# Kernel optimization log

Hardware: AMD Instinct MI355X
Metric: run time of the kernel (lower is better)

Reference implementation:

```python
import jax, jax.numpy as jnp
import numpy as np

EMB = 1024
HEADS = 16
HEAD_SZ = EMB // HEADS
EPS = 1e-5


def _layernorm(x, g, b):
    mu = jnp.mean(x, axis=-1, keepdims=True)
    var = jnp.mean(jnp.square(x - mu), axis=-1, keepdims=True)
    return (x - mu) * jax.lax.rsqrt(var + EPS) * g + b


def setup_inputs() -> dict:
    key = jax.random.key(0)
    ks = jax.random.split(key, 12)
    s_in = 1.0 / np.sqrt(EMB)
    s_h = 1.0 / np.sqrt(4 * EMB)
    return {
        "x": jax.random.normal(ks[0], (4, 1024, EMB), jnp.float32),
        # per-head Q/K/V projections stacked: [H, EMB, HEAD_SZ], no bias
        "wq": jax.random.normal(ks[1], (HEADS, EMB, HEAD_SZ), jnp.float32) * s_in,
        "wk": jax.random.normal(ks[2], (HEADS, EMB, HEAD_SZ), jnp.float32) * s_in,
        "wv": jax.random.normal(ks[3], (HEADS, EMB, HEAD_SZ), jnp.float32) * s_in,
        "w_proj": jax.random.normal(ks[4], (EMB, EMB), jnp.float32) * s_in,
        "b_proj": jnp.zeros((EMB,), jnp.float32),
        "w1": jax.random.normal(ks[5], (EMB, 4 * EMB), jnp.float32) * s_in,
        "b1": jnp.zeros((4 * EMB,), jnp.float32),
        "w2": jax.random.normal(ks[6], (4 * EMB, EMB), jnp.float32) * s_h,
        "b2": jnp.zeros((EMB,), jnp.float32),
        "g1": jnp.ones((EMB,), jnp.float32),
        "be1": jnp.zeros((EMB,), jnp.float32),
        "g2": jnp.ones((EMB,), jnp.float32),
        "be2": jnp.zeros((EMB,), jnp.float32),
    }


def reference(x, wq, wk, wv, w_proj, b_proj, w1, b1, w2, b2, g1, be1, g2, be2):
    B, T, C = x.shape
    # --- self-attention (pre-norm) ---
    h = _layernorm(x, g1, be1)
    q = jnp.einsum("btc,hcd->bhtd", h, wq)
    k = jnp.einsum("btc,hcd->bhtd", h, wk)
    v = jnp.einsum("btc,hcd->bhtd", h, wv)
    scale = 1.0 / jnp.sqrt(jnp.asarray(HEAD_SZ, x.dtype))
    scores = jnp.einsum("bhtd,bhsd->bhts", q, k) * scale  # non-causal: SDPA called with no mask
    attn = jax.nn.softmax(scores, axis=-1)
    o = jnp.einsum("bhts,bhsd->bhtd", attn, v)
    o = o.transpose(0, 2, 1, 3).reshape(B, T, C)  # concat heads (same order as torch.cat)
    sa_out = o @ w_proj + b_proj
    x = x + sa_out
    # --- feed-forward; note ln2 applied twice, faithful to source ---
    t = _layernorm(x, g2, be2)
    t = _layernorm(t, g2, be2)
    ff = jax.nn.relu(t @ w1 + b1) @ w2 + b2
    return x + ff
```

## Files before the change

kernel.cpp:

```cpp
#include <hip/hip_runtime.h>
#include <hip/hip_bf16.h>
#include <math.h>
#include <stdint.h>

typedef __bf16 bf16_t;
typedef __bf16 bf16x4 __attribute__((ext_vector_type(4)));
typedef __bf16 bf16x8 __attribute__((ext_vector_type(8)));
typedef float floatx4 __attribute__((ext_vector_type(4)));

#define BM 128
#define BK 32

__device__ __forceinline__ void gload16(const void* g, void* lds) {
    __builtin_amdgcn_global_load_lds(
        (__attribute__((address_space(1))) void*)(uintptr_t)g,
        (__attribute__((address_space(3))) void*)(uintptr_t)lds,
        16, 0, 0);
}

__global__ void transpose_all(const float* __restrict__ wq, const float* __restrict__ wk,
                              const float* __restrict__ wv, const float* __restrict__ w_proj,
                              const float* __restrict__ w1, const float* __restrict__ w2,
                              bf16_t* __restrict__ WQKVT, bf16_t* __restrict__ WPROJT,
                              bf16_t* __restrict__ W1T, bf16_t* __restrict__ W2T)
{
    const int idx = blockIdx.x;
    const float* in; bf16_t* out; int R, C, rt, ct;
    if (idx < 768) {
        const int z = idx >> 8;
        const int hd = (idx >> 4) & 15;
        rt = idx & 15; ct = 0; R = 1024; C = 64;
        in  = (z == 0 ? wq : z == 1 ? wk : wv) + hd * 65536;
        out = WQKVT + z * (1 << 20) + hd * 65536;
    } else if (idx < 1024) {
        const int t = idx - 768; rt = t & 15; ct = t >> 4; R = 1024; C = 1024;
        in = w_proj; out = WPROJT;
    } else if (idx < 2048) {
        const int t = idx - 1024; rt = t & 15; ct = t >> 4; R = 1024; C = 4096;
        in = w1; out = W1T;
    } else {
        const int t = idx - 2048; rt = t & 63; ct = t >> 6; R = 4096; C = 1024;
        in = w2; out = W2T;
    }
    __shared__ float tile[64][65];
    const int tid = threadIdx.x;
    const int r0 = rt * 64, c0 = ct * 64;
    const int tr = tid >> 4;
    const int tc = (tid & 15) * 4;
#pragma unroll
    for (int rr = 0; rr < 4; rr++) {
        const int r = tr + rr * 16;
        const float4 v = *(const float4*)&in[(long)(r0 + r) * C + c0 + tc];
        tile[r][tc + 0] = v.x; tile[r][tc + 1] = v.y;
        tile[r][tc + 2] = v.z; tile[r][tc + 3] = v.w;
    }
    __syncthreads();
#pragma unroll
    for (int rr = 0; rr < 4; rr++) {
        const int c = tr + rr * 16;
        bf16x4 o;
        o[0] = (bf16_t)tile[tc + 0][c];
        o[1] = (bf16_t)tile[tc + 1][c];
        o[2] = (bf16_t)tile[tc + 2][c];
        o[3] = (bf16_t)tile[tc + 3][c];
        *(bf16x4*)&out[(long)(c0 + c) * R + r0 + tc] = o;
    }
}

__global__ void ln_kernel(const float* __restrict__ x, const float* __restrict__ g,
                          const float* __restrict__ b, bf16_t* __restrict__ outb)
{
    const int row = blockIdx.x;
    const int tid = threadIdx.x;
    const float4 v = ((const float4*)(x + (long)row * 1024))[tid];
    float s  = v.x + v.y + v.z + v.w;
    float s2 = v.x * v.x + v.y * v.y + v.z * v.z + v.w * v.w;
#pragma unroll
    for (int off = 32; off >= 1; off >>= 1) {
        s  += __shfl_xor(s, off);
        s2 += __shfl_xor(s2, off);
    }
    __shared__ float red[8];
    const int wv = tid >> 6;
    if ((tid & 63) == 0) { red[wv] = s; red[4 + wv] = s2; }
    __syncthreads();
    s  = red[0] + red[1] + red[2] + red[3];
    s2 = red[4] + red[5] + red[6] + red[7];
    const float mu  = s * (1.0f / 1024.0f);
    const float var = fmaxf(s2 * (1.0f / 1024.0f) - mu * mu, 0.0f);
    const float rs  = rsqrtf(var + 1e-5f);
    const float4 gv = ((const float4*)g)[tid];
    const float4 bv = ((const float4*)b)[tid];
    bf16x4 o;
    o[0] = (bf16_t)((v.x - mu) * rs * gv.x + bv.x);
    o[1] = (bf16_t)((v.y - mu) * rs * gv.y + bv.y);
    o[2] = (bf16_t)((v.z - mu) * rs * gv.z + bv.z);
    o[3] = (bf16_t)((v.w - mu) * rs * gv.w + bv.w);
    ((bf16x4*)(outb + (long)row * 1024))[tid] = o;
}

__global__ void ln2x_kernel(const float* __restrict__ x, const float* __restrict__ g,
                            const float* __restrict__ b, bf16_t* __restrict__ outb)
{
    const int row = blockIdx.x;
    const int tid = threadIdx.x;
    const float4 v = ((const float4*)(x + (long)row * 1024))[tid];
    float s  = v.x + v.y + v.z + v.w;
    float s2 = v.x * v.x + v.y * v.y + v.z * v.z + v.w * v.w;
#pragma unroll
    for (int off = 32; off >= 1; off >>= 1) {
        s  += __shfl_xor(s, off);
        s2 += __shfl_xor(s2, off);
    }
    __shared__ float red[8];
    __shared__ float red2[8];
    const int wv = tid >> 6;
    if ((tid & 63) == 0) { red[wv] = s; red[4 + wv] = s2; }
    __syncthreads();
    s  = red[0] + red[1] + red[2] + red[3];
    s2 = red[4] + red[5] + red[6] + red[7];
    float mu  = s * (1.0f / 1024.0f);
    float var = fmaxf(s2 * (1.0f / 1024.0f) - mu * mu, 0.0f);
    float rs  = rsqrtf(var + 1e-5f);
    const float4 gv = ((const float4*)g)[tid];
    const float4 bv = ((const float4*)b)[tid];
    float y0 = (v.x - mu) * rs * gv.x + bv.x;
    float y1 = (v.y - mu) * rs * gv.y + bv.y;
    float y2 = (v.z - mu) * rs * gv.z + bv.z;
    float y3 = (v.w - mu) * rs * gv.w + bv.w;
    s  = y0 + y1 + y2 + y3;
    s2 = y0 * y0 + y1 * y1 + y2 * y2 + y3 * y3;
#pragma unroll
    for (int off = 32; off >= 1; off >>= 1) {
        s  += __shfl_xor(s, off);
        s2 += __shfl_xor(s2, off);
    }
    if ((tid & 63) == 0) { red2[wv] = s; red2[4 + wv] = s2; }
    __syncthreads();
    s  = red2[0] + red2[1] + red2[2] + red2[3];
    s2 = red2[4] + red2[5] + red2[6] + red2[7];
    mu  = s * (1.0f / 1024.0f);
    var = fmaxf(s2 * (1.0f / 1024.0f) - mu * mu, 0.0f);
    rs  = rsqrtf(var + 1e-5f);
    bf16x4 o;
    o[0] = (bf16_t)((y0 - mu) * rs * gv.x + bv.x);
    o[1] = (bf16_t)((y1 - mu) * rs * gv.y + bv.y);
    o[2] = (bf16_t)((y2 - mu) * rs * gv.z + bv.z);
    o[3] = (bf16_t)((y3 - mu) * rs * gv.w + bv.w);
    ((bf16x4*)(outb + (long)row * 1024))[tid] = o;
}

template<int EPI, int BNt>
__global__ __launch_bounds__(256, 2)
void gemm_bt(const bf16_t* __restrict__ A, const bf16_t* __restrict__ Bt,
             const int K,
             const float* __restrict__ bias, const float* __restrict__ resid,
             float* __restrict__ outf, bf16_t* __restrict__ outb,
             bf16_t* __restrict__ aux1, bf16_t* __restrict__ aux2,
             const int Nout)
{
    constexpr int NFRAG = BNt / 16;
    __shared__ __align__(16) bf16_t As[3][BM * BK];
    __shared__ __align__(16) bf16_t Bs[3][BNt * BK];
    const int tid  = threadIdx.x;
    const int wave = tid >> 6, lane = tid & 63;
    const int bm = blockIdx.x * BM, bn = blockIdx.y * BNt;

    floatx4 acc[2][NFRAG];
#pragma unroll
    for (int i = 0; i < 2; i++)
#pragma unroll
        for (int j = 0; j < NFRAG; j++) acc[i][j] = (floatx4){0.f, 0.f, 0.f, 0.f};

    const int srow  = lane >> 2;
    const int sbyte = (lane & 3) * 16;
    const char* gA0 = (const char*)(A + (size_t)(bm + wave * 32 + srow)      * K) + sbyte;
    const char* gA1 = (const char*)(A + (size_t)(bm + wave * 32 + 16 + srow) * K) + sbyte;
    const char* gB0;
    const char* gB1 = nullptr;
    if (BNt == 128) {
        gB0 = (const char*)(Bt + (size_t)(bn + wave * 32 + srow)      * K) + sbyte;
        gB1 = (const char*)(Bt + (size_t)(bn + wave * 32 + 16 + srow) * K) + sbyte;
    } else {
        gB0 = (const char*)(Bt + (size_t)(bn + wave * 16 + srow) * K) + sbyte;
    }
    const int laOff0 = (wave * 32) * 64;
    const int laOff1 = (wave * 32 + 16) * 64;
    const int lbOff0 = (BNt == 128) ? laOff0 : (wave * 16) * 64;

    const int fr = lane & 15;
    const int fk = (lane >> 4) * 8;

    auto stage = [&](int t, int bu) {
        const size_t kb = (size_t)t * (BK * 2);
        gload16(gA0 + kb, (char*)As[bu] + laOff0);
        gload16(gA1 + kb, (char*)As[bu] + laOff1);
        gload16(gB0 + kb, (char*)Bs[bu] + lbOff0);
        if (BNt == 128) gload16(gB1 + kb, (char*)Bs[bu] + laOff1);
    };

    auto compute = [&](int bu) {
        bf16x8 af[2], bfv[NFRAG];
#pragma unroll
        for (int i = 0; i < 2; i++)
            af[i] = *(const bf16x8*)&As[bu][(wave * 32 + i * 16 + fr) * BK + fk];
#pragma unroll
        for (int j = 0; j < NFRAG; j++)
            bfv[j] = *(const bf16x8*)&Bs[bu][(j * 16 + fr) * BK + fk];
#pragma unroll
        for (int i = 0; i < 2; i++)
#pragma unroll
            for (int j = 0; j < NFRAG; j++)
                acc[i][j] = __builtin_amdgcn_mfma_f32_16x16x32_bf16(af[i], bfv[j], acc[i][j], 0, 0, 0);
    };

    const int NT = K / BK;
    stage(0, 0);
    stage(1, 1);
    int bu = 0;
    for (int t = 0; t < NT - 1; ++t) {
        if (BNt == 128) asm volatile("s_waitcnt vmcnt(4)\n\ts_barrier" ::: "memory");
        else            asm volatile("s_waitcnt vmcnt(3)\n\ts_barrier" ::: "memory");
        if (t + 2 < NT) stage(t + 2, (t + 2) % 3);
        compute(bu);
        bu = (bu + 1) % 3;
    }
    asm volatile("s_waitcnt vmcnt(0)\n\ts_barrier" ::: "memory");
    compute(bu);

    const int er = (lane >> 4) * 4, ec = lane & 15;
#pragma unroll
    for (int i = 0; i < 2; i++) {
#pragma unroll
        for (int j = 0; j < NFRAG; j++) {
            const int col = bn + j * 16 + ec;
#pragma unroll
            for (int r = 0; r < 4; r++) {
                const int row = bm + wave * 32 + i * 16 + er + r;
                const float v = acc[i][j][r];
                if (EPI == 0) {
                    const int b = row >> 10, t = row & 1023;
                    if (col < 1024) {
                        const int h = col >> 6, d = col & 63;
                        outb[(size_t)((b * 16 + h) * 1024 + t) * 64 + d] = (bf16_t)v;
                    } else if (col < 2048) {
                        const int c2 = col - 1024, h = c2 >> 6, d = c2 & 63;
                        aux1[(size_t)((b * 16 + h) * 1024 + t) * 64 + d] = (bf16_t)v;
                    } else {
                        const int c2 = col - 2048, h = c2 >> 6, d = c2 & 63;
                        aux2[(size_t)((b * 16 + h) * 64 + d) * 1024 + t] = (bf16_t)v;
                    }
                } else if (EPI == 1 || EPI == 3) {
                    const size_t idx = (size_t)row * Nout + col;
                    outf[idx] = v + bias[col] + resid[idx];
                } else if (EPI == 2) {
                    const size_t idx = (size_t)row * Nout + col;
                    outb[idx] = (bf16_t)fmaxf(v + bias[col], 0.f);
                }
            }
        }
    }
}

__global__ __launch_bounds__(256, 4)
void attn_kernel(const bf16_t* __restrict__ Q, const bf16_t* __restrict__ Kg,
                 const bf16_t* __restrict__ Vt, bf16_t* __restrict__ Og)
{
    __shared__ __align__(16) bf16_t Ks[2][4096];
    __shared__ __align__(16) bf16_t Vs[2][4096];
    __shared__ __align__(16) bf16_t Ps[4][1024];
    const int tid = threadIdx.x, wave = tid >> 6, lane = tid & 63;
    const int bh = blockIdx.y;
    const int b = bh >> 4, h = bh & 15;
    const int q0 = blockIdx.x * 64 + wave * 16;
    const bf16_t* Qb = Q + (size_t)bh * 65536;
    const char* Kb = (const char*)(Kg + (size_t)bh * 65536);
    const char* Vb = (const char*)(Vt + (size_t)bh * 65536);
    const int fr = lane & 15, g = lane >> 4, fk = g * 8;

    const bf16x8 qf0 = *(const bf16x8*)&Qb[(size_t)(q0 + fr) * 64 + fk];
    const bf16x8 qf1 = *(const bf16x8*)&Qb[(size_t)(q0 + fr) * 64 + 32 + fk];

    floatx4 o[4];
#pragma unroll
    for (int dt = 0; dt < 4; dt++) o[dt] = (floatx4){0.f, 0.f, 0.f, 0.f};
    float lsum[4] = {0.f, 0.f, 0.f, 0.f};
    bf16_t* pw = &Ps[wave][0];
    const float sscale = 0.125f * 1.44269504088896f;

    auto stage = [&](int s0, int bu) {
#pragma unroll
        for (int t = 0; t < 2; t++) {
            const int j = wave * 2 + t;
            gload16(Kb + (size_t)(s0 + lane) * 128 + j * 16, &Ks[bu][j * 512]);
            gload16(Vb + (size_t)lane * 2048 + (size_t)s0 * 2 + j * 16, &Vs[bu][j * 512]);
        }
    };

    stage(0, 0);
    int bu = 0;
    for (int it = 0; it < 16; ++it) {
        __syncthreads();
        if (it < 15) stage((it + 1) * 64, bu ^ 1);
        const bf16_t* Kl = Ks[bu];
        const bf16_t* Vl = Vs[bu];

        floatx4 sacc[4];
#pragma unroll
        for (int ss = 0; ss < 4; ss++) sacc[ss] = (floatx4){0.f, 0.f, 0.f, 0.f};
#pragma unroll
        for (int c = 0; c < 2; c++) {
            const int ch = c * 4 + g;
            const bf16x8 qf = (c == 0) ? qf0 : qf1;
#pragma unroll
            for (int ss = 0; ss < 4; ss++) {
                const bf16x8 kf = *(const bf16x8*)&Kl[ch * 512 + (ss * 16 + fr) * 8];
                sacc[ss] = __builtin_amdgcn_mfma_f32_16x16x32_bf16(qf, kf, sacc[ss], 0, 0, 0);
            }
        }
#pragma unroll
        for (int ss = 0; ss < 4; ss++) {
#pragma unroll
            for (int r = 0; r < 4; r++) {
                const float p = __builtin_amdgcn_exp2f(sacc[ss][r] * sscale);
                lsum[r] += p;
                const int q = g * 4 + r;
                pw[(ss * 2 + (fr >> 3)) * 128 + q * 8 + (fr & 7)] = (bf16_t)p;
            }
        }
        asm volatile("s_waitcnt lgkmcnt(0)" ::: "memory");
#pragma unroll
        for (int c = 0; c < 2; c++) {
            const int ch = c * 4 + g;
            const bf16x8 pf = *(const bf16x8*)&pw[ch * 128 + fr * 8];
#pragma unroll
            for (int dt = 0; dt < 4; dt++) {
                const bf16x8 vf = *(const bf16x8*)&Vl[ch * 512 + (dt * 16 + fr) * 8];
                o[dt] = __builtin_amdgcn_mfma_f32_16x16x32_bf16(pf, vf, o[dt], 0, 0, 0);
            }
        }
        asm volatile("" ::: "memory");
        bu ^= 1;
    }
#pragma unroll
    for (int r = 0; r < 4; r++) {
        float l = lsum[r];
        l += __shfl_xor(l, 1);
        l += __shfl_xor(l, 2);
        l += __shfl_xor(l, 4);
        l += __shfl_xor(l, 8);
        lsum[r] = 1.0f / l;
    }
    const int t = q0 + g * 4;
#pragma unroll
    for (int dt = 0; dt < 4; dt++) {
#pragma unroll
        for (int r = 0; r < 4; r++) {
            const size_t idx = ((size_t)(b * 1024 + t + r)) * 1024 + h * 64 + dt * 16 + fr;
            Og[idx] = (bf16_t)(o[dt][r] * lsum[r]);
        }
    }
}

extern "C" void kernel_launch(void* const* d_in, const int* in_sizes, int n_in,
                              void* d_out, int out_size, void* d_ws, size_t ws_size,
                              hipStream_t stream)
{
    const float* x      = (const float*)d_in[0];
    const float* wq     = (const float*)d_in[1];
    const float* wk     = (const float*)d_in[2];
    const float* wv     = (const float*)d_in[3];
    const float* w_proj = (const float*)d_in[4];
    const float* b_proj = (const float*)d_in[5];
    const float* w1     = (const float*)d_in[6];
    const float* b1     = (const float*)d_in[7];
    const float* w2     = (const float*)d_in[8];
    const float* b2     = (const float*)d_in[9];
    const float* g1     = (const float*)d_in[10];
    const float* be1    = (const float*)d_in[11];
    const float* g2     = (const float*)d_in[12];
    const float* be2    = (const float*)d_in[13];
    float* out = (float*)d_out;
    char* ws = (char*)d_ws;

    bf16_t* WQKVT = (bf16_t*)(ws + 0x0000000);
    bf16_t* WPROJT= (bf16_t*)(ws + 0x0600000);
    bf16_t* W1T   = (bf16_t*)(ws + 0x0800000);
    bf16_t* W2T   = (bf16_t*)(ws + 0x1000000);
    bf16_t* HB    = (bf16_t*)(ws + 0x1800000);
    bf16_t* Qb    = (bf16_t*)(ws + 0x2000000);
    bf16_t* Kb    = (bf16_t*)(ws + 0x2800000);
    bf16_t* Vtb   = (bf16_t*)(ws + 0x3000000);
    bf16_t* AO    = (bf16_t*)(ws + 0x3800000);
    float*  X2    = (float*)(ws + 0x4000000);
    bf16_t* TB    = (bf16_t*)(ws + 0x2800000);
    bf16_t* FF1B  = (bf16_t*)(ws + 0x5000000);

    dim3 blk(256);
    transpose_all<<<3072, blk, 0, stream>>>(wq, wk, wv, w_proj, w1, w2,
                                            WQKVT, WPROJT, W1T, W2T);
    ln_kernel<<<4096, blk, 0, stream>>>(x, g1, be1, HB);
    gemm_bt<0, 128><<<dim3(32, 24), blk, 0, stream>>>(HB, WQKVT, 1024, nullptr, nullptr,
                                                      nullptr, Qb, Kb, Vtb, 3072);
    attn_kernel<<<dim3(16, 64), blk, 0, stream>>>(Qb, Kb, Vtb, AO);
    gemm_bt<1, 64><<<dim3(32, 16), blk, 0, stream>>>(AO, WPROJT, 1024, b_proj, x,
                                                     X2, nullptr, nullptr, nullptr, 1024);
    ln2x_kernel<<<4096, blk, 0, stream>>>(X2, g2, be2, TB);
    gemm_bt<2, 128><<<dim3(32, 32), blk, 0, stream>>>(TB, W1T, 1024, b1, nullptr,
                                                      nullptr, FF1B, nullptr, nullptr, 4096);
    gemm_bt<3, 64><<<dim3(32, 16), blk, 0, stream>>>(FF1B, W2T, 4096, b2, X2,
                                                     out, nullptr, nullptr, nullptr, 1024);
}
```

Before: 324.6 us.

## Replace direct global-to-LDS triple buffering with register-staged double buffering

The GEMM main loop no longer uses global_load_lds into a three-deep LDS ring. It now loads tiles into registers two steps ahead and writes them into a two-buffer LDS ping-pong, with lgkmcnt waits and barriers between stages. This halves LDS use per block and gives the compiler control over load scheduling, which may help occupancy. The cost is extra VGPRs for the staging slots, explicit ds_write instructions, and a risk of exposed global load latency, since the compiler inserts vmcnt waits before each store.

```diff
diff --git a/kernel.cpp b/kernel.cpp
--- a/kernel.cpp
+++ b/kernel.cpp
@@ -160,8 +160,8 @@
              const int Nout)
 {
     constexpr int NFRAG = BNt / 16;
-    __shared__ __align__(16) bf16_t As[3][BM * BK];
-    __shared__ __align__(16) bf16_t Bs[3][BNt * BK];
+    __shared__ __align__(16) bf16_t As[2][BM * BK];
+    __shared__ __align__(16) bf16_t Bs[2][BNt * BK];
     const int tid  = threadIdx.x;
     const int wave = tid >> 6, lane = tid & 63;
     const int bm = blockIdx.x * BM, bn = blockIdx.y * BNt;
@@ -173,32 +173,41 @@
         for (int j = 0; j < NFRAG; j++) acc[i][j] = (floatx4){0.f, 0.f, 0.f, 0.f};
 
     const int srow  = lane >> 2;
-    const int sbyte = (lane & 3) * 16;
-    const char* gA0 = (const char*)(A + (size_t)(bm + wave * 32 + srow)      * K) + sbyte;
-    const char* gA1 = (const char*)(A + (size_t)(bm + wave * 32 + 16 + srow) * K) + sbyte;
-    const char* gB0;
-    const char* gB1 = nullptr;
+    const int selem = (lane & 3) * 8;
+    const bf16_t* gA0 = A + (size_t)(bm + wave * 32 + srow)      * K + selem;
+    const bf16_t* gA1 = A + (size_t)(bm + wave * 32 + 16 + srow) * K + selem;
+    const bf16_t* gB0;
+    const bf16_t* gB1 = nullptr;
     if (BNt == 128) {
-        gB0 = (const char*)(Bt + (size_t)(bn + wave * 32 + srow)      * K) + sbyte;
-        gB1 = (const char*)(Bt + (size_t)(bn + wave * 32 + 16 + srow) * K) + sbyte;
+        gB0 = Bt + (size_t)(bn + wave * 32 + srow)      * K + selem;
+        gB1 = Bt + (size_t)(bn + wave * 32 + 16 + srow) * K + selem;
     } else {
-        gB0 = (const char*)(Bt + (size_t)(bn + wave * 16 + srow) * K) + sbyte;
-    }
-    const int laOff0 = (wave * 32) * 64;
-    const int laOff1 = (wave * 32 + 16) * 64;
-    const int lbOff0 = (BNt == 128) ? laOff0 : (wave * 16) * 64;
+        gB0 = Bt + (size_t)(bn + wave * 16 + srow) * K + selem;
+    }
+    const int wA0 = (wave * 32 + srow) * BK + selem;
+    const int wA1 = (wave * 32 + 16 + srow) * BK + selem;
+    const int wB0 = (BNt == 128) ? wA0 : (wave * 16 + srow) * BK + selem;
+    const int wB1 = wA1;
 
     const int fr = lane & 15;
     const int fk = (lane >> 4) * 8;
 
-    auto stage = [&](int t, int bu) {
-        const size_t kb = (size_t)t * (BK * 2);
-        gload16(gA0 + kb, (char*)As[bu] + laOff0);
-        gload16(gA1 + kb, (char*)As[bu] + laOff1);
-        gload16(gB0 + kb, (char*)Bs[bu] + lbOff0);
-        if (BNt == 128) gload16(gB1 + kb, (char*)Bs[bu] + laOff1);
+    struct Slot { uint4 a0, a1, b0, b1; };
+    Slot s0, s1;
+
+    auto load = [&](Slot& s, int t) {
+        const size_t off = (size_t)t * BK;
+        s.a0 = *(const uint4*)(gA0 + off);
+        s.a1 = *(const uint4*)(gA1 + off);
+        s.b0 = *(const uint4*)(gB0 + off);
+        if (BNt == 128) s.b1 = *(const uint4*)(gB1 + off);
     };
-
+    auto store = [&](const Slot& s, int bu) {
+        *(uint4*)&As[bu][wA0] = s.a0;
+        *(uint4*)&As[bu][wA1] = s.a1;
+        *(uint4*)&Bs[bu][wB0] = s.b0;
+        if (BNt == 128) *(uint4*)&Bs[bu][wB1] = s.b1;
+    };
     auto compute = [&](int bu) {
         bf16x8 af[2], bfv[NFRAG];
 #pragma unroll
@@ -215,18 +224,22 @@
     };
 
     const int NT = K / BK;
-    stage(0, 0);
-    stage(1, 1);
-    int bu = 0;
-    for (int t = 0; t < NT - 1; ++t) {
-        if (BNt == 128) asm volatile("s_waitcnt vmcnt(4)\n\ts_barrier" ::: "memory");
-        else            asm volatile("s_waitcnt vmcnt(3)\n\ts_barrier" ::: "memory");
-        if (t + 2 < NT) stage(t + 2, (t + 2) % 3);
-        compute(bu);
-        bu = (bu + 1) % 3;
-    }
-    asm volatile("s_waitcnt vmcnt(0)\n\ts_barrier" ::: "memory");
-    compute(bu);
+    load(s1, 0);
+    load(s0, 1);
+    store(s1, 0);
+    asm volatile("s_waitcnt lgkmcnt(0)\n\ts_barrier" ::: "memory");
+    for (int t = 0; t < NT; t += 2) {
+        if (t + 2 < NT) load(s1, t + 2);
+        compute(0);
+        store(s0, 1);
+        asm volatile("s_waitcnt lgkmcnt(0)\n\ts_barrier" ::: "memory");
+        if (t + 3 < NT) load(s0, t + 3);
+        compute(1);
+        if (t + 2 < NT) {
+            store(s1, 0);
+            asm volatile("s_waitcnt lgkmcnt(0)\n\ts_barrier" ::: "memory");
+        }
+    }
 
     const int er = (lane >> 4) * 4, ec = lane & 15;
 #pragma unroll
```

Result: slower. 730.7 us (+125.1%).
